# Kernel tuning notes

Measured on AMD Instinct MI355X. Metric: run time of the kernel, lower is better.

Reference implementation:

```python
import jax, jax.numpy as jnp
import numpy as np


def setup_inputs() -> dict:
    key = jax.random.key(0)
    k1, k2 = jax.random.split(key)
    B, T, D, E = 4, 4096, 2048, 64
    x = jax.random.normal(k1, (B, T, D), dtype=jnp.float32)
    # nn.Linear default init ~ U(-1/sqrt(D), 1/sqrt(D)); scaled normal is fine for a numeric baseline
    W = jax.random.normal(k2, (D, E), dtype=jnp.float32) * (1.0 / np.sqrt(D))
    b = jnp.zeros((E,), dtype=jnp.float32)
    return {"x": x, "W": W, "b": b}


TOPK = 2


def reference(x, W, b):
    # logits: (B, T, E)
    logits = jnp.einsum("btd,de->bte", x, W) + b
    probs = jax.nn.softmax(logits, axis=-1)
    topk_vals, topk_idx = jax.lax.top_k(probs, TOPK)
    return topk_idx, topk_vals
```

## Files before the change

### kernel.cpp

```cpp
#include <hip/hip_runtime.h>
#include <math.h>


#define D_DIM 2048
#define E_DIM 64
#define M_DIM 16384
#define BK 32
#define NCHUNK (D_DIM / BK)

typedef _Float16 half8 __attribute__((ext_vector_type(8)));
typedef float floatx4 __attribute__((ext_vector_type(4)));

__global__ __launch_bounds__(256) void split_w_kernel(
    const float* __restrict__ Wm, _Float16* __restrict__ wsT)
{
    __shared__ float t[64][65];
    const int tid = threadIdx.x;
    const int k0  = blockIdx.x * 64;

    #pragma unroll
    for (int p = 0; p < 16; p++) {
        int i  = p * 256 + tid;
        int kk = i >> 6, n = i & 63;
        t[n][kk] = Wm[(size_t)(k0 + kk) * E_DIM + n];
    }
    __syncthreads();
    #pragma unroll
    for (int p = 0; p < 16; p++) {
        int i  = p * 256 + tid;
        int kk = i & 63, n = i >> 6;
        float v = t[n][kk];
        _Float16 h = (_Float16)v;
        _Float16 l = (_Float16)((v - (float)h) * 2048.0f);
        wsT[(size_t)n * D_DIM + k0 + kk]            = h;
        wsT[(size_t)(E_DIM + n) * D_DIM + k0 + kk]  = l;
    }
}

__global__ __launch_bounds__(256) void router_mfma_kernel(
    const float* __restrict__ x, const _Float16* __restrict__ wsT,
    const float* __restrict__ bias, float* __restrict__ out)
{
    const int lane = threadIdx.x & 63;
    const int wave = threadIdx.x >> 6;
    const int c    = lane & 15;
    const int quad = lane >> 4;
    const int r0   = blockIdx.x * 64 + wave * 16;

    const float* xp = x + (size_t)(r0 + c) * D_DIM + quad * 8;
    const _Float16* whp = wsT + (size_t)c * D_DIM + quad * 8;
    const _Float16* wlp = whp + (size_t)E_DIM * D_DIM;

    floatx4 accm[4] = {};
    floatx4 accl[4] = {};

    float4 xs0[2], xs1[2], xs2[2], xs3[2];
    half8  wh0[4], wl0[4], wh1[4], wl1[4];

    auto loadx = [&](int ch, float4* dst) {
        const int kk = ch < NCHUNK ? ch : NCHUNK - 1;
        const float* p = xp + kk * BK;
        dst[0] = *reinterpret_cast<const float4*>(p);
        dst[1] = *reinterpret_cast<const float4*>(p + 4);
    };
    auto loadw = [&](int ch, half8* h, half8* l) {
        const int kk = ch < NCHUNK ? ch : NCHUNK - 1;
        #pragma unroll
        for (int t = 0; t < 4; t++) {
            h[t] = *reinterpret_cast<const half8*>(whp + (size_t)t * 16 * D_DIM + kk * BK);
            l[t] = *reinterpret_cast<const half8*>(wlp + (size_t)t * 16 * D_DIM + kk * BK);
        }
    };
    auto compute = [&](const float4* xs, const half8* h, const half8* l) {
        const float xv[8] = {xs[0].x, xs[0].y, xs[0].z, xs[0].w,
                             xs[1].x, xs[1].y, xs[1].z, xs[1].w};
        half8 ah, al;
        #pragma unroll
        for (int j = 0; j < 8; j++) {
            _Float16 hh = (_Float16)xv[j];
            ah[j] = hh;
            al[j] = (_Float16)((xv[j] - (float)hh) * 2048.0f);
        }
        #pragma unroll
        for (int t = 0; t < 4; t++) {
            accm[t] = __builtin_amdgcn_mfma_f32_16x16x32_f16(ah, h[t], accm[t], 0, 0, 0);
            accl[t] = __builtin_amdgcn_mfma_f32_16x16x32_f16(al, h[t], accl[t], 0, 0, 0);
            accl[t] = __builtin_amdgcn_mfma_f32_16x16x32_f16(ah, l[t], accl[t], 0, 0, 0);
        }
    };

    loadx(0, xs0); loadx(1, xs1); loadw(0, wh0, wl0);

    #pragma unroll 1
    for (int ch = 0; ch < NCHUNK; ch += 4) {
        loadx(ch + 2, xs2); loadw(ch + 1, wh1, wl1);
        compute(xs0, wh0, wl0);
        loadx(ch + 3, xs3); loadw(ch + 2, wh0, wl0);
        compute(xs1, wh1, wl1);
        loadx(ch + 4, xs0); loadw(ch + 3, wh1, wl1);
        compute(xs2, wh0, wl0);
        loadx(ch + 5, xs1); loadw(ch + 4, wh0, wl0);
        compute(xs3, wh1, wl1);
    }

    const float scale = 1.0f / 2048.0f;
    float bvt[4];
    #pragma unroll
    for (int t = 0; t < 4; t++) bvt[t] = bias[c + 16 * t];

    #pragma unroll
    for (int i = 0; i < 4; i++) {
        const float l0 = accm[0][i] + accl[0][i] * scale + bvt[0];
        const float l1 = accm[1][i] + accl[1][i] * scale + bvt[1];
        const float l2 = accm[2][i] + accl[2][i] * scale + bvt[2];
        const float l3 = accm[3][i] + accl[3][i] * scale + bvt[3];

        float m = fmaxf(fmaxf(l0, l1), fmaxf(l2, l3));
        #pragma unroll
        for (int off = 1; off < 16; off <<= 1)
            m = fmaxf(m, __shfl_xor(m, off, 64));

        const float e0 = expf(l0 - m), e1 = expf(l1 - m);
        const float e2 = expf(l2 - m), e3 = expf(l3 - m);
        float s = e0 + e1 + e2 + e3;
        #pragma unroll
        for (int off = 1; off < 16; off <<= 1)
            s += __shfl_xor(s, off, 64);

        const float p0 = e0 / s, p1 = e1 / s, p2 = e2 / s, p3 = e3 / s;

        const unsigned long long ka =
            ((unsigned long long)__float_as_uint(p0) << 32) | (unsigned long long)(63 - c);
        const unsigned long long kb =
            ((unsigned long long)__float_as_uint(p1) << 32) | (unsigned long long)(47 - c);
        const unsigned long long kc_ =
            ((unsigned long long)__float_as_uint(p2) << 32) | (unsigned long long)(31 - c);
        const unsigned long long kd =
            ((unsigned long long)__float_as_uint(p3) << 32) | (unsigned long long)(15 - c);

        unsigned long long hi1 = ka > kb ? ka : kb, lo1 = ka > kb ? kb : ka;
        unsigned long long hi2 = kc_ > kd ? kc_ : kd, lo2 = kc_ > kd ? kd : kc_;
        unsigned long long k1 = hi1 > hi2 ? hi1 : hi2;
        unsigned long long mn = hi1 > hi2 ? hi2 : hi1;
        unsigned long long mx = lo1 > lo2 ? lo1 : lo2;
        unsigned long long k2 = mn > mx ? mn : mx;

        #pragma unroll
        for (int off = 1; off < 16; off <<= 1) {
            const unsigned long long o1 = __shfl_xor(k1, off, 64);
            const unsigned long long o2 = __shfl_xor(k2, off, 64);
            const unsigned long long n1 = k1 > o1 ? k1 : o1;
            const unsigned long long w1 = k1 > o1 ? o1 : k1;
            const unsigned long long w2 = k2 > o2 ? k2 : o2;
            k1 = n1;
            k2 = w1 > w2 ? w1 : w2;
        }

        if (c == 0) {
            const int gr = r0 + 4 * quad + i;
            out[gr * 2 + 0] = (float)(63 - (int)(k1 & 0xFFFFFFFFull));
            out[gr * 2 + 1] = (float)(63 - (int)(k2 & 0xFFFFFFFFull));
            out[M_DIM * 2 + gr * 2 + 0] = __uint_as_float((unsigned)(k1 >> 32));
            out[M_DIM * 2 + gr * 2 + 1] = __uint_as_float((unsigned)(k2 >> 32));
        }
    }
}

extern "C" void kernel_launch(void* const* d_in, const int* in_sizes, int n_in,
                              void* d_out, int out_size, void* d_ws, size_t ws_size,
                              hipStream_t stream) {
    const float* x  = (const float*)d_in[0];
    const float* Wm = (const float*)d_in[1];
    const float* b  = (const float*)d_in[2];
    float* out = (float*)d_out;
    _Float16* wsT = (_Float16*)d_ws;

    split_w_kernel<<<dim3(D_DIM / 64), dim3(256), 0, stream>>>(Wm, wsT);
    router_mfma_kernel<<<dim3(M_DIM / 64), dim3(256), 0, stream>>>(x, wsT, b, out);
}
```

Measured before the change: 239.1 us.

## Split the K dimension across waves and reduce partial logits in shared memory

Each block now handles 16 rows instead of 64, and its four waves each accumulate a quarter of the 2048-long reduction dimension. The partial logits are summed through an LDS buffer before wave 0 runs softmax and top-2. This quadruples the grid to 1024 blocks and shortens each wave's serial K loop, aiming for more parallelism and latency hiding on a bandwidth-bound read of x. It adds an LDS reduction and a barrier, and leaves three of the four waves idle during the epilogue. The launch bounds also gain a minimum-occupancy hint of four blocks.

```diff
diff --git a/kernel.cpp b/kernel.cpp
--- a/kernel.cpp
+++ b/kernel.cpp
@@ -6,7 +6,8 @@
 #define E_DIM 64
 #define M_DIM 16384
 #define BK 32
-#define NCHUNK (D_DIM / BK)
+#define KSEG (D_DIM / 4)
+#define NCH  (KSEG / BK)
 
 typedef _Float16 half8 __attribute__((ext_vector_type(8)));
 typedef float floatx4 __attribute__((ext_vector_type(4)));
@@ -32,12 +33,12 @@
         float v = t[n][kk];
         _Float16 h = (_Float16)v;
         _Float16 l = (_Float16)((v - (float)h) * 2048.0f);
-        wsT[(size_t)n * D_DIM + k0 + kk]            = h;
-        wsT[(size_t)(E_DIM + n) * D_DIM + k0 + kk]  = l;
+        wsT[(size_t)n * D_DIM + k0 + kk]           = h;
+        wsT[(size_t)(E_DIM + n) * D_DIM + k0 + kk] = l;
     }
 }
 
-__global__ __launch_bounds__(256) void router_mfma_kernel(
+__global__ __launch_bounds__(256, 4) void router_mfma_kernel(
     const float* __restrict__ x, const _Float16* __restrict__ wsT,
     const float* __restrict__ bias, float* __restrict__ out)
 {
@@ -45,10 +46,11 @@
     const int wave = threadIdx.x >> 6;
     const int c    = lane & 15;
     const int quad = lane >> 4;
-    const int r0   = blockIdx.x * 64 + wave * 16;
+    const int r0   = blockIdx.x * 16;
+    const int kb   = wave * KSEG;
 
-    const float* xp = x + (size_t)(r0 + c) * D_DIM + quad * 8;
-    const _Float16* whp = wsT + (size_t)c * D_DIM + quad * 8;
+    const float* xp = x + (size_t)(r0 + c) * D_DIM + kb + quad * 8;
+    const _Float16* whp = wsT + (size_t)c * D_DIM + kb + quad * 8;
     const _Float16* wlp = whp + (size_t)E_DIM * D_DIM;
 
     floatx4 accm[4] = {};
@@ -58,13 +60,13 @@
     half8  wh0[4], wl0[4], wh1[4], wl1[4];
 
     auto loadx = [&](int ch, float4* dst) {
-        const int kk = ch < NCHUNK ? ch : NCHUNK - 1;
+        const int kk = ch < NCH ? ch : NCH - 1;
         const float* p = xp + kk * BK;
         dst[0] = *reinterpret_cast<const float4*>(p);
         dst[1] = *reinterpret_cast<const float4*>(p + 4);
     };
     auto loadw = [&](int ch, half8* h, half8* l) {
-        const int kk = ch < NCHUNK ? ch : NCHUNK - 1;
+        const int kk = ch < NCH ? ch : NCH - 1;
         #pragma unroll
         for (int t = 0; t < 4; t++) {
             h[t] = *reinterpret_cast<const half8*>(whp + (size_t)t * 16 * D_DIM + kk * BK);
@@ -92,7 +94,7 @@
     loadx(0, xs0); loadx(1, xs1); loadw(0, wh0, wl0);
 
     #pragma unroll 1
-    for (int ch = 0; ch < NCHUNK; ch += 4) {
+    for (int ch = 0; ch < NCH; ch += 4) {
         loadx(ch + 2, xs2); loadw(ch + 1, wh1, wl1);
         compute(xs0, wh0, wl0);
         loadx(ch + 3, xs3); loadw(ch + 2, wh0, wl0);
@@ -103,17 +105,32 @@
         compute(xs3, wh1, wl1);
     }
 
+    __shared__ float red[4][16][65];
     const float scale = 1.0f / 2048.0f;
+    #pragma unroll
+    for (int t = 0; t < 4; t++)
+        #pragma unroll
+        for (int i = 0; i < 4; i++)
+            red[wave][quad * 4 + i][c + 16 * t] = accm[t][i] + accl[t][i] * scale;
+    __syncthreads();
+
+    if (wave != 0) return;
+
     float bvt[4];
     #pragma unroll
     for (int t = 0; t < 4; t++) bvt[t] = bias[c + 16 * t];
 
     #pragma unroll
     for (int i = 0; i < 4; i++) {
-        const float l0 = accm[0][i] + accl[0][i] * scale + bvt[0];
-        const float l1 = accm[1][i] + accl[1][i] * scale + bvt[1];
-        const float l2 = accm[2][i] + accl[2][i] * scale + bvt[2];
-        const float l3 = accm[3][i] + accl[3][i] * scale + bvt[3];
+        const int row = quad * 4 + i;
+        float lt[4];
+        #pragma unroll
+        for (int t = 0; t < 4; t++) {
+            const int col = c + 16 * t;
+            lt[t] = red[0][row][col] + red[1][row][col]
+                  + red[2][row][col] + red[3][row][col] + bvt[t];
+        }
+        const float l0 = lt[0], l1 = lt[1], l2 = lt[2], l3 = lt[3];
 
         float m = fmaxf(fmaxf(l0, l1), fmaxf(l2, l3));
         #pragma unroll
@@ -131,14 +148,14 @@
 
         const unsigned long long ka =
             ((unsigned long long)__float_as_uint(p0) << 32) | (unsigned long long)(63 - c);
-        const unsigned long long kb =
+        const unsigned long long kb_ =
             ((unsigned long long)__float_as_uint(p1) << 32) | (unsigned long long)(47 - c);
         const unsigned long long kc_ =
             ((unsigned long long)__float_as_uint(p2) << 32) | (unsigned long long)(31 - c);
         const unsigned long long kd =
             ((unsigned long long)__float_as_uint(p3) << 32) | (unsigned long long)(15 - c);
 
-        unsigned long long hi1 = ka > kb ? ka : kb, lo1 = ka > kb ? kb : ka;
+        unsigned long long hi1 = ka > kb_ ? ka : kb_, lo1 = ka > kb_ ? kb_ : ka;
         unsigned long long hi2 = kc_ > kd ? kc_ : kd, lo2 = kc_ > kd ? kd : kc_;
         unsigned long long k1 = hi1 > hi2 ? hi1 : hi2;
         unsigned long long mn = hi1 > hi2 ? hi2 : hi1;
@@ -157,7 +174,7 @@
         }
 
         if (c == 0) {
-            const int gr = r0 + 4 * quad + i;
+            const int gr = r0 + row;
             out[gr * 2 + 0] = (float)(63 - (int)(k1 & 0xFFFFFFFFull));
             out[gr * 2 + 1] = (float)(63 - (int)(k2 & 0xFFFFFFFFull));
             out[M_DIM * 2 + gr * 2 + 0] = __uint_as_float((unsigned)(k1 >> 32));
@@ -176,5 +193,5 @@
     _Float16* wsT = (_Float16*)d_ws;
 
     split_w_kernel<<<dim3(D_DIM / 64), dim3(256), 0, stream>>>(Wm, wsT);
-    router_mfma_kernel<<<dim3(M_DIM / 64), dim3(256), 0, stream>>>(x, wsT, b, out);
+    router_mfma_kernel<<<dim3(M_DIM / 16), dim3(256), 0, stream>>>(x, wsT, b, out);
 }
```

After: 260.5 us. 9.0% more time.
